# Performance work log

Hardware: AMD Instinct MI355X
Metric: run time of the kernel (lower is better)

Reference implementation:

```python
import jax, jax.numpy as jnp
import numpy as np

WS = 16          # window_size
OWS = 24         # overlap_win_size = int(16*0.5) + 16
NH = 6           # num_heads
DIM = 192
HD = DIM // NH   # head_dim = 32
PAD = (OWS - WS) // 2


def _ln(x, g, b, eps=1e-5):
    mu = x.mean(-1, keepdims=True)
    var = ((x - mu) ** 2).mean(-1, keepdims=True)
    return (x - mu) * jax.lax.rsqrt(var + eps) * g + b


def _rel_bias(table):
    # relative position index between ws x ws queries and ows x ows keys
    cq = jnp.stack(jnp.meshgrid(jnp.arange(WS), jnp.arange(WS), indexing='ij')).reshape(2, -1)
    ck = jnp.stack(jnp.meshgrid(jnp.arange(OWS), jnp.arange(OWS), indexing='ij')).reshape(2, -1)
    rel = cq[:, :, None] - ck[:, None, :] + (OWS - 1)   # [2, S, Sk]
    idx = rel[0] * (WS + OWS - 1) + rel[1]               # [S, Sk]
    return table[idx].transpose(2, 0, 1)                 # [nh, S, Sk]


def setup_inputs() -> dict:
    key = jax.random.key(0)
    ks = jax.random.split(key, 8)
    c, hid = DIM, int(DIM * 2.0)
    std = 0.02
    return {
        'x': jax.random.normal(ks[0], (4, 128 * 128, c), jnp.float32),
        'norm1_g': jnp.ones((c,), jnp.float32),
        'norm1_b': jnp.zeros((c,), jnp.float32),
        'qkv_w': jax.random.normal(ks[1], (c, 3 * c), jnp.float32) * std,
        'qkv_b': jnp.zeros((3 * c,), jnp.float32),
        'rpb_table': jax.random.normal(ks[2], ((WS + OWS - 1) ** 2, NH), jnp.float32) * std,
        'proj_w': jax.random.normal(ks[3], (c, c), jnp.float32) * std,
        'proj_b': jnp.zeros((c,), jnp.float32),
        'norm2_g': jnp.ones((c,), jnp.float32),
        'norm2_b': jnp.zeros((c,), jnp.float32),
        'fc1_w': jax.random.normal(ks[4], (c, hid), jnp.float32) * std,
        'fc1_b': jnp.zeros((hid,), jnp.float32),
        'fc2_w': jax.random.normal(ks[5], (hid, c), jnp.float32) * std,
        'fc2_b': jnp.zeros((c,), jnp.float32),
        'h': 128,
        'w': 128,
    }


def reference(x, norm1_g, norm1_b, qkv_w, qkv_b, rpb_table, proj_w, proj_b,
              norm2_g, norm2_b, fc1_w, fc1_b, fc2_w, fc2_b, h, w):
    b, L, c = x.shape
    nwh, nww = h // WS, w // WS
    shortcut = x

    xn = _ln(x, norm1_g, norm1_b).reshape(b, h, w, c)
    qkv = xn @ qkv_w + qkv_b                       # [b, h, w, 3c]
    q, kf, vf = qkv[..., :c], qkv[..., c:2 * c], qkv[..., 2 * c:]

    # non-overlapping query windows -> [b*nw, nh, ws*ws, hd]
    q = q.reshape(b, nwh, WS, nww, WS, c).transpose(0, 1, 3, 2, 4, 5)
    q = q.reshape(-1, WS * WS, NH, HD).transpose(0, 2, 1, 3)

    # overlapping KV windows via zero-padded gather (== nn.Unfold(k=OWS, s=WS, p=PAD))
    kv = jnp.concatenate([kf, vf], axis=-1)        # [b, h, w, 2c]
    kv = jnp.pad(kv, ((0, 0), (PAD, PAD), (PAD, PAD), (0, 0)))
    ih = jnp.arange(nwh)[:, None] * WS + jnp.arange(OWS)[None, :]   # [nwh, OWS]
    iw = jnp.arange(nww)[:, None] * WS + jnp.arange(OWS)[None, :]
    p = kv[:, ih]                                  # [b, nwh, OWS, Wp, 2c]
    p = p[:, :, :, iw]                             # [b, nwh, OWS, nww, OWS, 2c]
    p = p.transpose(0, 1, 3, 2, 4, 5).reshape(-1, OWS * OWS, 2 * c)
    k = p[..., :c].reshape(-1, OWS * OWS, NH, HD).transpose(0, 2, 1, 3)
    v = p[..., c:].reshape(-1, OWS * OWS, NH, HD).transpose(0, 2, 1, 3)

    scale = HD ** -0.5
    attn = jnp.einsum('wnqd,wnkd->wnqk', q * scale, k) + _rel_bias(rpb_table)[None]
    attn = jax.nn.softmax(attn, axis=-1)
    o = jnp.einsum('wnqk,wnkd->wnqd', attn, v)     # [b*nw, nh, S, hd]
    o = o.transpose(0, 2, 1, 3).reshape(b, nwh, nww, WS, WS, c)
    o = o.transpose(0, 1, 3, 2, 4, 5).reshape(b, h * w, c)   # window_reverse

    x = shortcut + (o @ proj_w + proj_b)
    y = _ln(x, norm2_g, norm2_b)
    y = jax.nn.gelu(y @ fc1_w + fc1_b, approximate=False)
    return x + (y @ fc2_w + fc2_b)
```

## Files before the change

### kernel.cpp

```cpp
#include <hip/hip_runtime.h>

using u16    = unsigned short;
using bf16x8 = __attribute__((ext_vector_type(8))) short;
using bf16x4 = __attribute__((ext_vector_type(4))) short;
using f32x4  = __attribute__((ext_vector_type(4))) float;
using i32x4  = __attribute__((ext_vector_type(4))) int;
using i32x2  = __attribute__((ext_vector_type(2))) int;

#define QSCALE 0.2550351115f
#define LOG2E  1.4426950408889634f

__device__ __forceinline__ u16 f2b(float f) {
  unsigned u = __builtin_bit_cast(unsigned, f);
  u = (u + 0x7fffu + ((u >> 16) & 1u)) >> 16;
  return (u16)u;
}
__device__ __forceinline__ float b2f(u16 h) {
  return __builtin_bit_cast(float, ((unsigned)h) << 16);
}
__device__ __forceinline__ int cvt_pk(float a, float b) {
  int r;
  asm("v_cvt_pk_bf16_f32 %0, %1, %2" : "=v"(r) : "v"(a), "v"(b));
  return r;
}
__device__ __forceinline__ void gload_lds16(const u16* g, u16* l) {
  __builtin_amdgcn_global_load_lds(
      (const __attribute__((address_space(1))) unsigned int*)(g),
      (__attribute__((address_space(3))) unsigned int*)(l), 16, 0, 0);
}

__global__ __launch_bounds__(256) void wconv_kernel(const float* __restrict__ src,
                                                    u16* __restrict__ dst, int K, int N) {
  __shared__ u16 tile[32][33];
  int kb = blockIdx.x * 32, nb = blockIdx.y * 32;
  int tx = threadIdx.x & 31, ty = threadIdx.x >> 5;
#pragma unroll
  for (int r = 0; r < 32; r += 8)
    tile[ty + r][tx] = f2b(src[(size_t)(kb + ty + r) * N + nb + tx]);
  __syncthreads();
#pragma unroll
  for (int r = 0; r < 32; r += 8)
    dst[(size_t)(nb + ty + r) * K + kb + tx] = tile[tx][ty + r];
}

__global__ void bias_pack_kernel(const float* __restrict__ table, float* __restrict__ biaspf) {
  int bid = blockIdx.x;
  int h = bid / 36, kt = bid - h * 36;
  int t = threadIdx.x;
  int w = t >> 6, lo = t & 15, lg = (t >> 4) & 3;
  float out[8];
#pragma unroll
  for (int qc = 0; qc < 2; ++qc)
#pragma unroll
    for (int r = 0; r < 4; ++r) {
      int q = w * 32 + qc * 16 + lo;
      int k = kt * 16 + lg * 4 + r;
      int i = q >> 4, j = q & 15;
      int oi = k / 24, oj = k - oi * 24;
      int idx = (i - oi + 23) * 39 + (j - oj + 23);
      out[qc * 4 + r] = table[idx * 6 + h] * LOG2E;
    }
  float* dst = biaspf + ((size_t)(bid * 512 + t)) * 8;
  *(f32x4*)dst       = *(const f32x4*)out;
  *(f32x4*)(dst + 4) = *(const f32x4*)(out + 4);
}

template <typename TI>
__global__ __launch_bounds__(256) void ln_kernel(const TI* __restrict__ xin,
                                                 const float* __restrict__ g,
                                                 const float* __restrict__ b,
                                                 u16* __restrict__ out) {
  int row = blockIdx.x * 4 + (threadIdx.x >> 6);
  int l = threadIdx.x & 63;
  const TI* xr = xin + (size_t)row * 192;
  float v0, v1, v2;
  if constexpr (sizeof(TI) == 2) {
    v0 = b2f(xr[l]); v1 = b2f(xr[l + 64]); v2 = b2f(xr[l + 128]);
  } else {
    v0 = xr[l]; v1 = xr[l + 64]; v2 = xr[l + 128];
  }
  float s1 = v0 + v1 + v2;
  float s2 = v0 * v0 + v1 * v1 + v2 * v2;
#pragma unroll
  for (int off = 32; off; off >>= 1) {
    s1 += __shfl_xor(s1, off);
    s2 += __shfl_xor(s2, off);
  }
  float mu = s1 * (1.0f / 192.0f);
  float var = s2 * (1.0f / 192.0f) - mu * mu;
  float rs = rsqrtf(var + 1e-5f);
  u16* orow = out + (size_t)row * 192;
  orow[l]       = f2b((v0 - mu) * rs * g[l]       + b[l]);
  orow[l + 64]  = f2b((v1 - mu) * rs * g[l + 64]  + b[l + 64]);
  orow[l + 128] = f2b((v2 - mu) * rs * g[l + 128] + b[l + 128]);
}

template <int N, int K, int EPI>
__global__ __launch_bounds__(256, 2) void gemm_kernel(
    const u16* __restrict__ A, const u16* __restrict__ WT,
    const float* __restrict__ bias, const void* __restrict__ res,
    void* __restrict__ outp) {
  __shared__ u16 As[128 * 192];
  __shared__ u16 Ws[64 * 192];
  const int t = threadIdx.x;
  const int l = t & 63, w = t >> 6;
  const int lo = l & 15, lg = l >> 4;
  constexpr int nbn = N / 64;
  const int bid = blockIdx.x;
  const int cpx = gridDim.x >> 3;
  const int wk = (bid & 7) * cpx + (bid >> 3);
  const int bm0 = (wk / nbn) * 128, bn0 = (wk % nbn) * 64;
  const int wr = (w >> 1) * 64, wc = (w & 1) * 32;
  f32x4 acc[4][2] = {};
  for (int c0 = 0; c0 < K; c0 += 192) {
    if (c0) __syncthreads();
#pragma unroll
    for (int i = 0; i < 12; ++i) {
      int u = t + i * 256;
      int row = u / 24, ch = u - row * 24;
      int cg = (ch & ~7) | ((ch ^ row) & 7);
      gload_lds16(&A[(size_t)(bm0 + row) * K + c0 + cg * 8], &As[u * 8]);
    }
#pragma unroll
    for (int i = 0; i < 6; ++i) {
      int u = t + i * 256;
      int row = u / 24, ch = u - row * 24;
      int cg = (ch & ~7) | ((ch ^ row) & 7);
      gload_lds16(&WT[(size_t)(bn0 + row) * K + c0 + cg * 8], &Ws[u * 8]);
    }
    __syncthreads();
#pragma unroll
    for (int kk = 0; kk < 6; ++kk) {
      int cb = kk * 4 + lg;
      int cofs = ((cb & ~7) | ((cb ^ lo) & 7)) * 8;
      bf16x8 b0 = *(const bf16x8*)&Ws[(wc + lo) * 192 + cofs];
      bf16x8 b1 = *(const bf16x8*)&Ws[(wc + 16 + lo) * 192 + cofs];
#pragma unroll
      for (int mi = 0; mi < 4; ++mi) {
        bf16x8 a = *(const bf16x8*)&As[(wr + mi * 16 + lo) * 192 + cofs];
        acc[mi][0] = __builtin_amdgcn_mfma_f32_16x16x32_bf16(a, b0, acc[mi][0], 0, 0, 0);
        acc[mi][1] = __builtin_amdgcn_mfma_f32_16x16x32_bf16(a, b1, acc[mi][1], 0, 0, 0);
      }
    }
  }
#pragma unroll
  for (int ni = 0; ni < 2; ++ni) {
    int n = bn0 + wc + ni * 16 + lo;
    float bs = bias[n];
#pragma unroll
    for (int mi = 0; mi < 4; ++mi)
#pragma unroll
      for (int r = 0; r < 4; ++r) {
        int m = bm0 + wr + mi * 16 + lg * 4 + r;
        float v = acc[mi][ni][r] + bs;
        size_t idx = (size_t)m * N + n;
        if constexpr (EPI == 2) {
          float gg = 0.5f * v * (1.0f + erff(v * 0.70710678118654752f));
          ((u16*)outp)[idx] = f2b(gg);
        } else if constexpr (EPI == 3) {
          float sc = (n < 192) ? QSCALE : 1.0f;
          ((u16*)outp)[idx] = f2b(v * sc);
        } else if constexpr (EPI == 4) {
          ((u16*)outp)[idx] = f2b(v + ((const float*)res)[idx]);
        } else {
          ((float*)outp)[idx] = v + b2f(((const u16*)res)[idx]);
        }
      }
  }
}

__global__ __launch_bounds__(512, 4) void attn_kernel(const u16* __restrict__ qkv,
                                                      const float* __restrict__ biaspf,
                                                      u16* __restrict__ o_out) {
  __shared__ u16 Kl[576 * 36];
  __shared__ u16 VT[32 * 600];
  const int bid = blockIdx.x;
  const int wk = (bid & 7) * 192 + (bid >> 3);
  const int h = wk % 6;
  const int wid = wk / 6;
  const int bb = wid >> 6, wy = (wid >> 3) & 7, wx = wid & 7;
  const int t = threadIdx.x;
  const int w = t >> 6, lo = t & 15, lg = (t >> 4) & 3;

#pragma unroll
  for (int i2 = 0; i2 < 5; ++i2) {
    int u = t + i2 * 512;
    if (u < 2304) {
      int pos = u >> 2, d0 = (u & 3) * 8;
      int oi = pos / 24, oj = pos - oi * 24;
      int y = wy * 16 - 4 + oi, x = wx * 16 - 4 + oj;
      i32x4 kv = {0, 0, 0, 0};
      bf16x8 vv = {0, 0, 0, 0, 0, 0, 0, 0};
      if ((unsigned)y < 128u && (unsigned)x < 128u) {
        const u16* s = qkv + (size_t)((bb << 14) + y * 128 + x) * 576 + h * 32 + d0;
        kv = *(const i32x4*)(s + 192);
        vv = *(const bf16x8*)(s + 384);
      }
      i32x2 klo = {kv[0], kv[1]}, khi = {kv[2], kv[3]};
      *(i32x2*)&Kl[pos * 36 + d0]     = klo;
      *(i32x2*)&Kl[pos * 36 + d0 + 4] = khi;
      int p5 = pos & 31;
      int slot = (((p5 >> 2) & 3) << 3) | (((p5 >> 4) & 1) << 2) | (p5 & 3);
      int base = (pos & ~31);
#pragma unroll
      for (int j = 0; j < 8; ++j) {
        int row = d0 + j;
        int scol = (slot & 7) | ((((slot >> 3) ^ (row >> 3)) & 3) << 3);
        VT[row * 600 + base + scol] = (u16)vv[j];
      }
    }
  }

  bf16x8 qf[2];
#pragma unroll
  for (int qc = 0; qc < 2; ++qc) {
    int yy = wy * 16 + w * 2 + qc, xx = wx * 16 + lo;
    qf[qc] = *(const bf16x8*)(qkv + (size_t)((bb << 14) + yy * 128 + xx) * 576 + h * 32 + lg * 8);
  }
  __syncthreads();

  float ls[2] = {0.0f, 0.0f};
  f32x4 oacc[2][2] = {};
  const f32x4* bbase = (const f32x4*)(biaspf + ((size_t)(h * 36) * 512 + t) * 8);
  f32x4 bc[4];
#pragma unroll
  for (int i = 0; i < 4; ++i) bc[i] = bbase[(i >> 1) * 1024 + (i & 1)];
  const int xr0 = lo >> 3, xr1 = 2 | (lo >> 3);

  for (int kt2 = 0; kt2 < 18; ++kt2) {
    int ktn = (kt2 < 17) ? (kt2 + 1) : 17;
    f32x4 bn[4];
#pragma unroll
    for (int i = 0; i < 4; ++i) bn[i] = bbase[(2 * ktn + (i >> 1)) * 1024 + (i & 1)];

    i32x4 pw[2];
#pragma unroll
    for (int hf = 0; hf < 2; ++hf) {
      int kt = kt2 * 2 + hf;
      int krow = (kt * 16 + lo) * 36 + lg * 8;
      bf16x4 k0 = *(const bf16x4*)&Kl[krow];
      bf16x4 k1 = *(const bf16x4*)&Kl[krow + 4];
      bf16x8 kf = {k0[0], k0[1], k0[2], k0[3], k1[0], k1[1], k1[2], k1[3]};
#pragma unroll
      for (int qc = 0; qc < 2; ++qc) {
        f32x4 c = __builtin_amdgcn_mfma_f32_16x16x32_bf16(kf, qf[qc], bc[hf * 2 + qc], 0, 0, 0);
        float p0 = __builtin_amdgcn_exp2f(c[0]);
        float p1 = __builtin_amdgcn_exp2f(c[1]);
        float p2 = __builtin_amdgcn_exp2f(c[2]);
        float p3 = __builtin_amdgcn_exp2f(c[3]);
        ls[qc] += (p0 + p1) + (p2 + p3);
        pw[qc][hf * 2 + 0] = cvt_pk(p0, p1);
        pw[qc][hf * 2 + 1] = cvt_pk(p2, p3);
      }
    }
    int vb = kt2 * 32;
    bf16x8 vb0 = *(const bf16x8*)&VT[lo * 600 + vb + ((lg ^ xr0) & 3) * 8];
    bf16x8 vb1 = *(const bf16x8*)&VT[(16 + lo) * 600 + vb + ((lg ^ xr1) & 3) * 8];
#pragma unroll
    for (int qc = 0; qc < 2; ++qc) {
      bf16x8 pa = __builtin_bit_cast(bf16x8, pw[qc]);
      oacc[qc][0] = __builtin_amdgcn_mfma_f32_16x16x32_bf16(pa, vb0, oacc[qc][0], 0, 0, 0);
      oacc[qc][1] = __builtin_amdgcn_mfma_f32_16x16x32_bf16(pa, vb1, oacc[qc][1], 0, 0, 0);
    }
#pragma unroll
    for (int i = 0; i < 4; ++i) bc[i] = bn[i];
  }

#pragma unroll
  for (int qc = 0; qc < 2; ++qc) {
    float s = ls[qc];
    s += __shfl_xor(s, 16);
    s += __shfl_xor(s, 32);
    float linv = 1.0f / s;
#pragma unroll
    for (int r = 0; r < 4; ++r) {
      float lv = __shfl(linv, lg * 4 + r);
      int yy = wy * 16 + w * 2 + qc, xx = wx * 16 + lg * 4 + r;
      u16* dst = o_out + (size_t)((bb << 14) + yy * 128 + xx) * 192 + h * 32 + lo;
      dst[0]  = f2b(oacc[qc][0][r] * lv);
      dst[16] = f2b(oacc[qc][1][r] * lv);
    }
  }
}

extern "C" void kernel_launch(void* const* d_in, const int* in_sizes, int n_in,
                              void* d_out, int out_size, void* d_ws, size_t ws_size,
                              hipStream_t stream) {
  (void)in_sizes; (void)n_in; (void)out_size; (void)ws_size;
  const float* x      = (const float*)d_in[0];
  const float* n1g    = (const float*)d_in[1];
  const float* n1b    = (const float*)d_in[2];
  const float* qkv_w  = (const float*)d_in[3];
  const float* qkv_b  = (const float*)d_in[4];
  const float* rpb    = (const float*)d_in[5];
  const float* proj_w = (const float*)d_in[6];
  const float* proj_b = (const float*)d_in[7];
  const float* n2g    = (const float*)d_in[8];
  const float* n2b    = (const float*)d_in[9];
  const float* fc1_w  = (const float*)d_in[10];
  const float* fc1_b  = (const float*)d_in[11];
  const float* fc2_w  = (const float*)d_in[12];
  const float* fc2_b  = (const float*)d_in[13];

  char* ws = (char*)d_ws;
  u16*   wq     = (u16*)(ws + 0);
  u16*   wp     = (u16*)(ws + 221184);
  u16*   wf1    = (u16*)(ws + 294912);
  u16*   wf2    = (u16*)(ws + 442368);
  float* biaspf = (float*)(ws + 589824);
  u16*   xnbuf  = (u16*)(ws + 4194304);
  u16*   qkvbuf = (u16*)(ws + 29360128);
  u16*   ybuf   = (u16*)(ws + 54525952);
  u16*   x2     = (u16*)(ws + 104857600);

  wconv_kernel<<<dim3(6, 18), 256, 0, stream>>>(qkv_w, wq, 192, 576);
  wconv_kernel<<<dim3(6, 6),  256, 0, stream>>>(proj_w, wp, 192, 192);
  wconv_kernel<<<dim3(6, 12), 256, 0, stream>>>(fc1_w, wf1, 192, 384);
  wconv_kernel<<<dim3(12, 6), 256, 0, stream>>>(fc2_w, wf2, 384, 192);
  bias_pack_kernel<<<216, 512, 0, stream>>>(rpb, biaspf);

  ln_kernel<float><<<16384, 256, 0, stream>>>(x, n1g, n1b, xnbuf);
  gemm_kernel<576, 192, 3><<<4608, 256, 0, stream>>>(xnbuf, wq, qkv_b, nullptr, qkvbuf);
  attn_kernel<<<1536, 512, 0, stream>>>(qkvbuf, biaspf, xnbuf);
  gemm_kernel<192, 192, 4><<<1536, 256, 0, stream>>>(xnbuf, wp, proj_b, x, x2);
  ln_kernel<u16><<<16384, 256, 0, stream>>>(x2, n2g, n2b, qkvbuf);
  gemm_kernel<384, 192, 2><<<3072, 256, 0, stream>>>(qkvbuf, wf1, fc1_b, nullptr, ybuf);
  gemm_kernel<192, 384, 5><<<1536, 256, 0, stream>>>(ybuf, wf2, fc2_b, x2, (float*)d_out);
}
```

Measured before the change: 313.9 us.

## Fuse LayerNorms into adjacent GEMMs and keep A tile resident across N tiles

Fuses LayerNorm1 into the QKV GEMM prologue and LayerNorm2 into the projection GEMM epilogue, with a cross-wave row reduction through shared memory. The QKV and fc1 GEMMs now keep one 128-row A tile resident in LDS and loop over all N tiles, restaging only the weight tile each time. This removes two standalone LN kernels and their intermediate HBM round-trips, and avoids reloading A for every N tile. In exchange, each of these fused kernels launches only 512 blocks, which lowers parallelism, and the per-tile weight staging is serialized between syncs rather than overlapped with compute.

```diff
diff --git a/kernel.cpp b/kernel.cpp
--- a/kernel.cpp
+++ b/kernel.cpp
@@ -65,34 +65,234 @@
   *(f32x4*)(dst + 4) = *(const f32x4*)(out + 4);
 }
 
-template <typename TI>
-__global__ __launch_bounds__(256) void ln_kernel(const TI* __restrict__ xin,
-                                                 const float* __restrict__ g,
-                                                 const float* __restrict__ b,
-                                                 u16* __restrict__ out) {
-  int row = blockIdx.x * 4 + (threadIdx.x >> 6);
-  int l = threadIdx.x & 63;
-  const TI* xr = xin + (size_t)row * 192;
-  float v0, v1, v2;
-  if constexpr (sizeof(TI) == 2) {
-    v0 = b2f(xr[l]); v1 = b2f(xr[l + 64]); v2 = b2f(xr[l + 128]);
+template <int N, int EPI, bool LNIN>
+__global__ __launch_bounds__(256, 2) void gemm_as_kernel(
+    const void* __restrict__ Ap, const u16* __restrict__ WT,
+    const float* __restrict__ bias, const float* __restrict__ lng,
+    const float* __restrict__ lnb, u16* __restrict__ outp) {
+  constexpr int AST = LNIN ? 200 : 192;
+  __shared__ u16 As[128 * AST];
+  __shared__ u16 Ws[64 * 192];
+  const int t = threadIdx.x;
+  const int l = t & 63, w = t >> 6;
+  const int lo = l & 15, lg = l >> 4;
+  const int m0 = blockIdx.x * 128;
+  const int wr = (w >> 1) * 64, wc = (w & 1) * 32;
+
+  if constexpr (LNIN) {
+    const float* A = (const float*)Ap;
+    float ga = lng[l], gb = lng[l + 64], gc = lng[l + 128];
+    float ba = lnb[l], bb = lnb[l + 64], bc = lnb[l + 128];
+    for (int rb = 0; rb < 32; rb += 8) {
+      float vv[8][3];
+#pragma unroll
+      for (int rr = 0; rr < 8; ++rr) {
+        int row = w * 32 + rb + rr;
+        const float* xr = A + (size_t)(m0 + row) * 192;
+        vv[rr][0] = xr[l]; vv[rr][1] = xr[l + 64]; vv[rr][2] = xr[l + 128];
+      }
+#pragma unroll
+      for (int rr = 0; rr < 8; ++rr) {
+        int row = w * 32 + rb + rr;
+        float s1 = vv[rr][0] + vv[rr][1] + vv[rr][2];
+        float s2 = vv[rr][0] * vv[rr][0] + vv[rr][1] * vv[rr][1] + vv[rr][2] * vv[rr][2];
+#pragma unroll
+        for (int off = 32; off; off >>= 1) {
+          s1 += __shfl_xor(s1, off);
+          s2 += __shfl_xor(s2, off);
+        }
+        float mu = s1 * (1.0f / 192.0f);
+        float var = s2 * (1.0f / 192.0f) - mu * mu;
+        float rs = rsqrtf(var + 1e-5f);
+        u16* ar = &As[row * 200];
+        ar[l]       = f2b((vv[rr][0] - mu) * rs * ga + ba);
+        ar[l + 64]  = f2b((vv[rr][1] - mu) * rs * gb + bb);
+        ar[l + 128] = f2b((vv[rr][2] - mu) * rs * gc + bc);
+      }
+    }
   } else {
-    v0 = xr[l]; v1 = xr[l + 64]; v2 = xr[l + 128];
-  }
-  float s1 = v0 + v1 + v2;
-  float s2 = v0 * v0 + v1 * v1 + v2 * v2;
-#pragma unroll
-  for (int off = 32; off; off >>= 1) {
-    s1 += __shfl_xor(s1, off);
-    s2 += __shfl_xor(s2, off);
-  }
-  float mu = s1 * (1.0f / 192.0f);
-  float var = s2 * (1.0f / 192.0f) - mu * mu;
-  float rs = rsqrtf(var + 1e-5f);
-  u16* orow = out + (size_t)row * 192;
-  orow[l]       = f2b((v0 - mu) * rs * g[l]       + b[l]);
-  orow[l + 64]  = f2b((v1 - mu) * rs * g[l + 64]  + b[l + 64]);
-  orow[l + 128] = f2b((v2 - mu) * rs * g[l + 128] + b[l + 128]);
+    const u16* A = (const u16*)Ap;
+#pragma unroll
+    for (int i = 0; i < 12; ++i) {
+      int u = t + i * 256;
+      int row = u / 24, ch = u - row * 24;
+      int cg = (ch & ~7) | ((ch ^ row) & 7);
+      gload_lds16(&A[(size_t)(m0 + row) * 192 + cg * 8], &As[u * 8]);
+    }
+  }
+
+  auto stageW = [&](int nt) {
+#pragma unroll
+    for (int i = 0; i < 6; ++i) {
+      int u = t + i * 256;
+      int row = u / 24, ch = u - row * 24;
+      int cg = (ch & ~7) | ((ch ^ row) & 7);
+      gload_lds16(&WT[(size_t)(nt * 64 + row) * 192 + cg * 8], &Ws[u * 8]);
+    }
+  };
+  stageW(0);
+  constexpr int NT = N / 64;
+  for (int nt = 0; nt < NT; ++nt) {
+    __syncthreads();
+    f32x4 acc[4][2] = {};
+#pragma unroll
+    for (int kk = 0; kk < 6; ++kk) {
+      int cb = kk * 4 + lg;
+      int cofs = ((cb & ~7) | ((cb ^ lo) & 7)) * 8;
+      bf16x8 wb0 = *(const bf16x8*)&Ws[(wc + lo) * 192 + cofs];
+      bf16x8 wb1 = *(const bf16x8*)&Ws[(wc + 16 + lo) * 192 + cofs];
+#pragma unroll
+      for (int mi = 0; mi < 4; ++mi) {
+        bf16x8 a;
+        if constexpr (LNIN) a = *(const bf16x8*)&As[(wr + mi * 16 + lo) * 200 + kk * 32 + lg * 8];
+        else                a = *(const bf16x8*)&As[(wr + mi * 16 + lo) * 192 + cofs];
+        acc[mi][0] = __builtin_amdgcn_mfma_f32_16x16x32_bf16(a, wb0, acc[mi][0], 0, 0, 0);
+        acc[mi][1] = __builtin_amdgcn_mfma_f32_16x16x32_bf16(a, wb1, acc[mi][1], 0, 0, 0);
+      }
+    }
+    __syncthreads();
+    if (nt + 1 < NT) stageW(nt + 1);
+#pragma unroll
+    for (int ni = 0; ni < 2; ++ni) {
+      int n = nt * 64 + wc + ni * 16 + lo;
+      float bs = bias[n];
+#pragma unroll
+      for (int mi = 0; mi < 4; ++mi)
+#pragma unroll
+        for (int r = 0; r < 4; ++r) {
+          int m = m0 + wr + mi * 16 + lg * 4 + r;
+          float v = acc[mi][ni][r] + bs;
+          if constexpr (EPI == 2)
+            v = 0.5f * v * (1.0f + erff(v * 0.70710678118654752f));
+          if constexpr (EPI == 3)
+            v *= (nt < 3) ? QSCALE : 1.0f;
+          outp[(size_t)m * N + n] = f2b(v);
+        }
+    }
+  }
+}
+
+__global__ __launch_bounds__(256, 2) void proj_ln_kernel(
+    const u16* __restrict__ o, const u16* __restrict__ WT,
+    const float* __restrict__ bias, const float* __restrict__ xres,
+    const float* __restrict__ g2, const float* __restrict__ b2,
+    u16* __restrict__ x2, u16* __restrict__ xn2) {
+  __shared__ u16 As[128 * 192];
+  __shared__ u16 Ws[64 * 192];
+  __shared__ float red[128][4];
+  const int t = threadIdx.x;
+  const int l = t & 63, w = t >> 6;
+  const int lo = l & 15, lg = l >> 4;
+  const int m0 = blockIdx.x * 128;
+  const int wr = (w >> 1) * 64, wc = (w & 1) * 32;
+
+#pragma unroll
+  for (int i = 0; i < 12; ++i) {
+    int u = t + i * 256;
+    int row = u / 24, ch = u - row * 24;
+    int cg = (ch & ~7) | ((ch ^ row) & 7);
+    gload_lds16(&o[(size_t)(m0 + row) * 192 + cg * 8], &As[u * 8]);
+  }
+  auto stageW = [&](int p) {
+#pragma unroll
+    for (int i = 0; i < 6; ++i) {
+      int u = t + i * 256;
+      int row = u / 24, ch = u - row * 24;
+      int cg = (ch & ~7) | ((ch ^ row) & 7);
+      gload_lds16(&WT[(size_t)(p * 64 + row) * 192 + cg * 8], &Ws[u * 8]);
+    }
+  };
+  stageW(0);
+  f32x4 acc[3][4][2] = {};
+#pragma unroll
+  for (int p = 0; p < 3; ++p) {
+    __syncthreads();
+#pragma unroll
+    for (int kk = 0; kk < 6; ++kk) {
+      int cb = kk * 4 + lg;
+      int cofs = ((cb & ~7) | ((cb ^ lo) & 7)) * 8;
+      bf16x8 wb0 = *(const bf16x8*)&Ws[(wc + lo) * 192 + cofs];
+      bf16x8 wb1 = *(const bf16x8*)&Ws[(wc + 16 + lo) * 192 + cofs];
+#pragma unroll
+      for (int mi = 0; mi < 4; ++mi) {
+        bf16x8 a = *(const bf16x8*)&As[(wr + mi * 16 + lo) * 192 + cofs];
+        acc[p][mi][0] = __builtin_amdgcn_mfma_f32_16x16x32_bf16(a, wb0, acc[p][mi][0], 0, 0, 0);
+        acc[p][mi][1] = __builtin_amdgcn_mfma_f32_16x16x32_bf16(a, wb1, acc[p][mi][1], 0, 0, 0);
+      }
+    }
+    __syncthreads();
+    if (p < 2) stageW(p + 1);
+  }
+
+  float bcol[3][2];
+#pragma unroll
+  for (int p = 0; p < 3; ++p)
+#pragma unroll
+    for (int ni = 0; ni < 2; ++ni) bcol[p][ni] = bias[p * 64 + wc + ni * 16 + lo];
+  float s1[4][4] = {}, s2[4][4] = {};
+#pragma unroll
+  for (int p = 0; p < 3; ++p)
+#pragma unroll
+    for (int ni = 0; ni < 2; ++ni) {
+      int col = p * 64 + wc + ni * 16 + lo;
+#pragma unroll
+      for (int mi = 0; mi < 4; ++mi)
+#pragma unroll
+        for (int r = 0; r < 4; ++r) {
+          int m = m0 + wr + mi * 16 + lg * 4 + r;
+          float v = acc[p][mi][ni][r] + bcol[p][ni] + xres[(size_t)m * 192 + col];
+          acc[p][mi][ni][r] = v;
+          s1[mi][r] += v;
+          s2[mi][r] += v * v;
+        }
+    }
+#pragma unroll
+  for (int mi = 0; mi < 4; ++mi)
+#pragma unroll
+    for (int r = 0; r < 4; ++r) {
+#pragma unroll
+      for (int off = 8; off; off >>= 1) {
+        s1[mi][r] += __shfl_xor(s1[mi][r], off);
+        s2[mi][r] += __shfl_xor(s2[mi][r], off);
+      }
+      if (lo == 0) {
+        int row = wr + mi * 16 + lg * 4 + r;
+        red[row][wc == 0 ? 0 : 2] = s1[mi][r];
+        red[row][wc == 0 ? 1 : 3] = s2[mi][r];
+      }
+    }
+  __syncthreads();
+
+  float gcol[3][2], b2col[3][2];
+#pragma unroll
+  for (int p = 0; p < 3; ++p)
+#pragma unroll
+    for (int ni = 0; ni < 2; ++ni) {
+      int col = p * 64 + wc + ni * 16 + lo;
+      gcol[p][ni] = g2[col];
+      b2col[p][ni] = b2[col];
+    }
+#pragma unroll
+  for (int mi = 0; mi < 4; ++mi)
+#pragma unroll
+    for (int r = 0; r < 4; ++r) {
+      int row = wr + mi * 16 + lg * 4 + r;
+      int m = m0 + row;
+      float S1 = red[row][0] + red[row][2];
+      float S2 = red[row][1] + red[row][3];
+      float mu = S1 * (1.0f / 192.0f);
+      float var = S2 * (1.0f / 192.0f) - mu * mu;
+      float rs = rsqrtf(var + 1e-5f);
+#pragma unroll
+      for (int p = 0; p < 3; ++p)
+#pragma unroll
+        for (int ni = 0; ni < 2; ++ni) {
+          int col = p * 64 + wc + ni * 16 + lo;
+          float v = acc[p][mi][ni][r];
+          x2[(size_t)m * 192 + col]  = f2b(v);
+          xn2[(size_t)m * 192 + col] = f2b((v - mu) * rs * gcol[p][ni] + b2col[p][ni]);
+        }
+    }
 }
 
 template <int N, int K, int EPI>
@@ -154,16 +354,10 @@
         int m = bm0 + wr + mi * 16 + lg * 4 + r;
         float v = acc[mi][ni][r] + bs;
         size_t idx = (size_t)m * N + n;
-        if constexpr (EPI == 2) {
-          float gg = 0.5f * v * (1.0f + erff(v * 0.70710678118654752f));
-          ((u16*)outp)[idx] = f2b(gg);
-        } else if constexpr (EPI == 3) {
-          float sc = (n < 192) ? QSCALE : 1.0f;
-          ((u16*)outp)[idx] = f2b(v * sc);
-        } else if constexpr (EPI == 4) {
-          ((u16*)outp)[idx] = f2b(v + ((const float*)res)[idx]);
+        if constexpr (EPI == 5) {
+          ((float*)outp)[idx] = v + b2f(((const u16*)res)[idx]);
         } else {
-          ((float*)outp)[idx] = v + b2f(((const u16*)res)[idx]);
+          ((u16*)outp)[idx] = f2b(v);
         }
       }
   }
@@ -308,10 +502,11 @@
   u16*   wf1    = (u16*)(ws + 294912);
   u16*   wf2    = (u16*)(ws + 442368);
   float* biaspf = (float*)(ws + 589824);
-  u16*   xnbuf  = (u16*)(ws + 4194304);
+  u16*   obuf   = (u16*)(ws + 4194304);
   u16*   qkvbuf = (u16*)(ws + 29360128);
-  u16*   ybuf   = (u16*)(ws + 54525952);
-  u16*   x2     = (u16*)(ws + 104857600);
+  u16*   ybuf   = (u16*)(ws + 29360128);
+  u16*   xn2    = (u16*)(ws + 104857600);
+  u16*   x2     = (u16*)(ws + 130023424);
 
   wconv_kernel<<<dim3(6, 18), 256, 0, stream>>>(qkv_w, wq, 192, 576);
   wconv_kernel<<<dim3(6, 6),  256, 0, stream>>>(proj_w, wp, 192, 192);
@@ -319,11 +514,9 @@
   wconv_kernel<<<dim3(12, 6), 256, 0, stream>>>(fc2_w, wf2, 384, 192);
   bias_pack_kernel<<<216, 512, 0, stream>>>(rpb, biaspf);
 
-  ln_kernel<float><<<16384, 256, 0, stream>>>(x, n1g, n1b, xnbuf);
-  gemm_kernel<576, 192, 3><<<4608, 256, 0, stream>>>(xnbuf, wq, qkv_b, nullptr, qkvbuf);
-  attn_kernel<<<1536, 512, 0, stream>>>(qkvbuf, biaspf, xnbuf);
-  gemm_kernel<192, 192, 4><<<1536, 256, 0, stream>>>(xnbuf, wp, proj_b, x, x2);
-  ln_kernel<u16><<<16384, 256, 0, stream>>>(x2, n2g, n2b, qkvbuf);
-  gemm_kernel<384, 192, 2><<<3072, 256, 0, stream>>>(qkvbuf, wf1, fc1_b, nullptr, ybuf);
+  gemm_as_kernel<576, 3, true><<<512, 256, 0, stream>>>(x, wq, qkv_b, n1g, n1b, qkvbuf);
+  attn_kernel<<<1536, 512, 0, stream>>>(qkvbuf, biaspf, obuf);
+  proj_ln_kernel<<<512, 256, 0, stream>>>(obuf, wp, proj_b, x, n2g, n2b, x2, xn2);
+  gemm_as_kernel<384, 2, false><<<512, 256, 0, stream>>>(xn2, wf1, fc1_b, nullptr, nullptr, ybuf);
   gemm_kernel<192, 384, 5><<<1536, 256, 0, stream>>>(ybuf, wf2, fc2_b, x2, (float*)d_out);
 }
```

Result: faster. 299.9 us (-4.5%).
